# Optimization experiments

Hardware: AMD Instinct MI355X
Metric: run time of the kernel (lower is better)

The kernel has to match this reference:

```python
import jax, jax.numpy as jnp
import numpy as np

S, B, D, H, L = 1024, 2, 1024, 16, 4
HD = D // H            # 64
MLP = 4 * D            # 4096
EPS = 1e-5


def _ln(x, w, b):
    m = x.mean(-1, keepdims=True)
    v = ((x - m) ** 2).mean(-1, keepdims=True)
    return (x - m) * jax.lax.rsqrt(v + EPS) * w + b


def _rotate_half(x):
    h = x.shape[-1] // 2
    return jnp.concatenate([-x[..., h:], x[..., :h]], axis=-1)


def _rope(t, cos, sin):
    # t: (B, S, H, HD); cos/sin: (S, HD) broadcast to (1, S, 1, HD)
    return t * cos[None, :, None, :] + _rotate_half(t) * sin[None, :, None, :]


def setup_inputs() -> dict:
    key = jax.random.key(0)
    ks = iter(jax.random.split(key, 64))

    def p(shape, scale=0.02):
        return jax.random.normal(next(ks), shape, jnp.float32) * scale

    return {
        "x": jax.random.normal(next(ks), (S, B, D), jnp.float32),
        "rotary_pos_emb": jax.random.normal(next(ks), (S, HD // 2), jnp.float32),
        # stacked per-layer params (leading dim L) for lax.scan
        "ln1_w": jnp.ones((L, D), jnp.float32), "ln1_b": jnp.zeros((L, D), jnp.float32),
        "in_w": p((L, 3 * D, D)), "in_b": jnp.zeros((L, 3 * D), jnp.float32),
        "out_w": p((L, D, D)), "out_b": jnp.zeros((L, D), jnp.float32),
        "ln2_w": jnp.ones((L, D), jnp.float32), "ln2_b": jnp.zeros((L, D), jnp.float32),
        "fc_w": p((L, MLP, D)), "fc_b": jnp.zeros((L, MLP), jnp.float32),
        "cp_w": p((L, D, MLP)), "cp_b": jnp.zeros((L, D), jnp.float32),
        # attention pooling head (qkv_bias=False in CrossAttention)
        "pn_q_w": jnp.ones((D,), jnp.float32), "pn_q_b": jnp.zeros((D,), jnp.float32),
        "pn_k_w": jnp.ones((D,), jnp.float32), "pn_k_b": jnp.zeros((D,), jnp.float32),
        "pn_v_w": jnp.ones((D,), jnp.float32), "pn_v_b": jnp.zeros((D,), jnp.float32),
        "pq_w": p((D, D)), "pk_w": p((D, D)), "pv_w": p((D, D)),
        "pp_w": p((D, D)), "pp_b": jnp.zeros((D,), jnp.float32),
    }


def reference(x, rotary_pos_emb, ln1_w, ln1_b, in_w, in_b, out_w, out_b,
              ln2_w, ln2_b, fc_w, fc_b, cp_w, cp_b,
              pn_q_w, pn_q_b, pn_k_w, pn_k_b, pn_v_w, pn_v_b,
              pq_w, pk_w, pv_w, pp_w, pp_b):
    # freqs (S, HD/2) -> cos/sin tiled twice along last dim: (S, HD)
    cos = jnp.tile(jnp.cos(rotary_pos_emb), (1, 2))
    sin = jnp.tile(jnp.sin(rotary_pos_emb), (1, 2))
    scale = 1.0 / np.sqrt(HD).astype(np.float32)

    def layer(h, p):
        l1w, l1b, iw, ib, ow, ob, l2w, l2b, fw, fb, cw, cb = p
        a = _ln(h, l1w, l1b)
        qkv = jnp.einsum('sbd,ed->sbe', a, iw) + ib           # (S,B,3D)
        qkv = qkv.reshape(S, B, 3, H, HD)
        q = jnp.transpose(qkv[:, :, 0], (1, 0, 2, 3))          # (B,S,H,HD)
        k = jnp.transpose(qkv[:, :, 1], (1, 0, 2, 3))
        v = jnp.transpose(qkv[:, :, 2], (1, 0, 2, 3))
        q = _rope(q, cos, sin)
        k = _rope(k, cos, sin)
        q, k, v = (t.transpose(0, 2, 1, 3) for t in (q, k, v))  # (B,H,S,HD)
        attn = jax.nn.softmax(jnp.einsum('bhsd,bhtd->bhst', q, k) * scale, axis=-1)
        o = jnp.einsum('bhst,bhtd->bhsd', attn, v)
        o = o.transpose(2, 0, 1, 3).reshape(S, B, D)           # back to (S,B,D)
        h = h + jnp.einsum('sbd,ed->sbe', o, ow) + ob          # residual + out_proj
        m = _ln(h, l2w, l2b)
        m = jax.nn.gelu(jnp.einsum('sbd,ed->sbe', m, fw) + fb, approximate=False)
        h = h + jnp.einsum('sbe,de->sbd', m, cw) + cb          # residual + c_proj
        return h, None

    h, _ = jax.lax.scan(layer, x, (ln1_w, ln1_b, in_w, in_b, out_w, out_b,
                                   ln2_w, ln2_b, fc_w, fc_b, cp_w, cp_b))

    # AttentionPoolingBlock: mean-pooled single query, cross-attend over tokens
    t = h.transpose(1, 0, 2)                                   # (B,N,C)
    xq = _ln(t.mean(1, keepdims=True), pn_q_w, pn_q_b)         # (B,1,C)
    xk = _ln(t, pn_k_w, pn_k_b)
    xv = _ln(t, pn_v_w, pn_v_b)
    q = (xq @ pq_w.T).reshape(B, 1, H, HD).transpose(0, 2, 1, 3)   # (B,H,1,HD)
    k = (xk @ pk_w.T).reshape(B, S, H, HD).transpose(0, 2, 1, 3)
    v = (xv @ pv_w.T).reshape(B, S, H, HD).transpose(0, 2, 1, 3)
    a = jax.nn.softmax(jnp.einsum('bhqd,bhtd->bhqt', q, k) * scale, axis=-1)
    o = jnp.einsum('bhqt,bhtd->bhqd', a, v).transpose(0, 2, 1, 3).reshape(B, 1, D)
    return (o @ pp_w.T + pp_b)[:, 0]                           # (B, D)
```

## Files before the change

kernel.cpp:

```cpp
#include <hip/hip_runtime.h>
#include <math.h>

#define S_LEN  1024
#define BATCH  2
#define DMODEL 1024
#define NHEAD  16
#define HDIM   64
#define NLAYER 4
#define MLPD   4096
#define MROWS  (S_LEN*BATCH)

typedef __attribute__((ext_vector_type(8))) short bf16x8_t;
typedef __attribute__((ext_vector_type(4))) float f32x4_t;

__device__ __forceinline__ unsigned short f2bf(float f) {
  union { float f; unsigned u; } c; c.f = f;
  return (unsigned short)((c.u + 0x7FFFu + ((c.u >> 16) & 1u)) >> 16);
}
__device__ __forceinline__ float bf2f(unsigned short u) {
  union { unsigned u; float f; } c; c.u = ((unsigned)u) << 16; return c.f;
}

__device__ __forceinline__ void gl_lds16(const unsigned short* g, unsigned short* l) {
  __builtin_amdgcn_global_load_lds(
      (const __attribute__((address_space(1))) unsigned int*)(g),
      (__attribute__((address_space(3))) unsigned int*)(l), 16, 0, 0);
}

template<int CTRL>
__device__ __forceinline__ float dpp16(float x) {
  return __int_as_float(__builtin_amdgcn_update_dpp(
      0, __float_as_int(x), CTRL, 0xf, 0xf, true));
}
__device__ __forceinline__ float rowmax16(float x) {
  x = fmaxf(x, dpp16<0x128>(x));
  x = fmaxf(x, dpp16<0x124>(x));
  x = fmaxf(x, dpp16<0x122>(x));
  x = fmaxf(x, dpp16<0x121>(x));
  return x;
}
__device__ __forceinline__ float rowsum16(float x) {
  x += dpp16<0x128>(x);
  x += dpp16<0x124>(x);
  x += dpp16<0x122>(x);
  x += dpp16<0x121>(x);
  return x;
}

__global__ __launch_bounds__(256) void w2bf_kernel(const float* __restrict__ src,
    unsigned short* __restrict__ dst, int n) {
  const int i = (blockIdx.x * 256 + threadIdx.x) * 8;
  if (i >= n) return;
  float4 v0 = *(const float4*)(src + i);
  float4 v1 = *(const float4*)(src + i + 4);
  ushort4 u0, u1;
  u0.x = f2bf(v0.x); u0.y = f2bf(v0.y); u0.z = f2bf(v0.z); u0.w = f2bf(v0.w);
  u1.x = f2bf(v1.x); u1.y = f2bf(v1.y); u1.z = f2bf(v1.z); u1.w = f2bf(v1.w);
  *(ushort4*)(dst + i)     = u0;
  *(ushort4*)(dst + i + 4) = u1;
}

__global__ __launch_bounds__(256) void trig_kernel(const float* __restrict__ rot,
    float2* __restrict__ tab) {
  const int i = blockIdx.x * 256 + threadIdx.x;
  const float f = rot[i];
  tab[i] = make_float2(cosf(f), sinf(f));
}

template<bool BF16OUT>
__global__ __launch_bounds__(256) void ln_kernel(const float* __restrict__ x,
    const float* __restrict__ w, const float* __restrict__ b,
    void* __restrict__ out, float inscale) {
  const int row = blockIdx.x;
  const int tid = threadIdx.x;
  const float* xr = x + (size_t)row * DMODEL;
  float4 v = *(const float4*)(xr + tid * 4);
  v.x *= inscale; v.y *= inscale; v.z *= inscale; v.w *= inscale;
  float s1 = v.x + v.y + v.z + v.w;
  float s2 = v.x*v.x + v.y*v.y + v.z*v.z + v.w*v.w;
  #pragma unroll
  for (int off = 32; off; off >>= 1) {
    s1 += __shfl_xor(s1, off);
    s2 += __shfl_xor(s2, off);
  }
  __shared__ float as1[4], as2[4];
  if ((tid & 63) == 0) { as1[tid >> 6] = s1; as2[tid >> 6] = s2; }
  __syncthreads();
  s1 = as1[0] + as1[1] + as1[2] + as1[3];
  s2 = as2[0] + as2[1] + as2[2] + as2[3];
  const float mean = s1 * (1.0f / DMODEL);
  const float var  = s2 * (1.0f / DMODEL) - mean * mean;
  const float r = rsqrtf(var + 1e-5f);
  float4 wv = *(const float4*)(w + tid * 4);
  float4 bv = *(const float4*)(b + tid * 4);
  float o0 = (v.x - mean) * r * wv.x + bv.x;
  float o1 = (v.y - mean) * r * wv.y + bv.y;
  float o2 = (v.z - mean) * r * wv.z + bv.z;
  float o3 = (v.w - mean) * r * wv.w + bv.w;
  if (BF16OUT) {
    ushort4 u; u.x = f2bf(o0); u.y = f2bf(o1); u.z = f2bf(o2); u.w = f2bf(o3);
    *(ushort4*)((unsigned short*)out + (size_t)row * DMODEL + tid * 4) = u;
  } else {
    float4 ov; ov.x = o0; ov.y = o1; ov.z = o2; ov.w = o3;
    *(float4*)((float*)out + (size_t)row * DMODEL + tid * 4) = ov;
  }
}

template<int NS, bool ADDDEST, bool DOLN>
__global__ __launch_bounds__(256) void reduce_ln_kernel(
    const float* __restrict__ part, const float* __restrict__ bias,
    float* __restrict__ dest, const float* __restrict__ lnw,
    const float* __restrict__ lnb, unsigned short* __restrict__ lnout) {
  const int row = blockIdx.x;
  const int tid = threadIdx.x;
  const size_t off = (size_t)row * DMODEL + tid * 4;
  float4 v;
  if (ADDDEST) v = *(const float4*)(dest + off);
  else { v.x = 0.f; v.y = 0.f; v.z = 0.f; v.w = 0.f; }
  if (bias) {
    float4 b4 = *(const float4*)(bias + tid * 4);
    v.x += b4.x; v.y += b4.y; v.z += b4.z; v.w += b4.w;
  }
  #pragma unroll
  for (int z = 0; z < NS; ++z) {
    float4 p = *(const float4*)(part + (size_t)z * (MROWS * DMODEL) + off);
    v.x += p.x; v.y += p.y; v.z += p.z; v.w += p.w;
  }
  *(float4*)(dest + off) = v;
  if (DOLN) {
    float s1 = v.x + v.y + v.z + v.w;
    float s2 = v.x*v.x + v.y*v.y + v.z*v.z + v.w*v.w;
    #pragma unroll
    for (int o = 32; o; o >>= 1) {
      s1 += __shfl_xor(s1, o);
      s2 += __shfl_xor(s2, o);
    }
    __shared__ float as1[4], as2[4];
    if ((tid & 63) == 0) { as1[tid >> 6] = s1; as2[tid >> 6] = s2; }
    __syncthreads();
    s1 = as1[0] + as1[1] + as1[2] + as1[3];
    s2 = as2[0] + as2[1] + as2[2] + as2[3];
    const float mean = s1 * (1.0f / DMODEL);
    const float var  = s2 * (1.0f / DMODEL) - mean * mean;
    const float r = rsqrtf(var + 1e-5f);
    float4 wv = *(const float4*)(lnw + tid * 4);
    float4 bv = *(const float4*)(lnb + tid * 4);
    ushort4 u;
    u.x = f2bf((v.x - mean) * r * wv.x + bv.x);
    u.y = f2bf((v.y - mean) * r * wv.y + bv.y);
    u.z = f2bf((v.z - mean) * r * wv.z + bv.z);
    u.w = f2bf((v.w - mean) * r * wv.w + bv.w);
    *(ushort4*)(lnout + (size_t)row * DMODEL + tid * 4) = u;
  }
}

template<int SPLIT, bool GELU, bool PARTIAL, bool OUTBF16>
__global__ __launch_bounds__(256, 3) void gemm_mfma(
    const unsigned short* __restrict__ A, const unsigned short* __restrict__ W,
    const float* __restrict__ bias, void* __restrict__ Cout,
    int M, int N, int K) {
  constexpr int BK = 32;
  __shared__ __align__(16) unsigned short As[2][128 * BK];
  __shared__ __align__(16) unsigned short Bs[2][128 * BK];
  const int tid  = threadIdx.x;
  const int wid  = tid >> 6;
  const int lane = tid & 63;
  const int lrow = lane & 15;
  const int lq   = lane >> 4;

  const int NB = gridDim.x, MB = gridDim.y;
  const int f = blockIdx.y * NB + blockIdx.x;
  const int xcd = f & 7;
  const int idx = f >> 3;
  const int m0 = (idx % MB) * 128;
  const int n0 = (xcd + (idx / MB) * 8) * 128;

  const int wm = (wid >> 1) * 64;
  const int wn = (wid & 1) * 64;
  const int Kc = K / SPLIT;
  const int kbase = blockIdx.z * Kc;

  f32x4_t acc[4][4];
  #pragma unroll
  for (int i = 0; i < 4; ++i)
    #pragma unroll
    for (int j = 0; j < 4; ++j) acc[i][j] = (f32x4_t){0.f, 0.f, 0.f, 0.f};

  const int c1 = tid, c2 = tid + 256;
  const int r1c = c1 >> 2, r2c = c2 >> 2;
  const int kc1 = ((c1 & 3) ^ ((r1c >> 1) & 3)) * 8;
  const int kc2 = ((c2 & 3) ^ ((r2c >> 1) & 3)) * 8;
  const unsigned short* Ag1 = A + (size_t)(m0 + r1c) * K + kbase + kc1;
  const unsigned short* Ag2 = A + (size_t)(m0 + r2c) * K + kbase + kc2;
  const unsigned short* Wg1 = W + (size_t)(n0 + r1c) * K + kbase + kc1;
  const unsigned short* Wg2 = W + (size_t)(n0 + r2c) * K + kbase + kc2;
  const int l1 = c1 * 8, l2 = c2 * 8;

  gl_lds16(Ag1, &As[0][l1]);
  gl_lds16(Ag2, &As[0][l2]);
  gl_lds16(Wg1, &Bs[0][l1]);
  gl_lds16(Wg2, &Bs[0][l2]);
  __syncthreads();

  int cur = 0;
  for (int k0 = 0; k0 < Kc; k0 += BK) {
    if (k0 + BK < Kc) {
      gl_lds16(Ag1 + k0 + BK, &As[cur ^ 1][l1]);
      gl_lds16(Ag2 + k0 + BK, &As[cur ^ 1][l2]);
      gl_lds16(Wg1 + k0 + BK, &Bs[cur ^ 1][l1]);
      gl_lds16(Wg2 + k0 + BK, &Bs[cur ^ 1][l2]);
    }

    bf16x8_t af[4], bfr[4];
    #pragma unroll
    for (int i = 0; i < 4; ++i) {
      const int row = wm + i * 16 + lrow;
      const int ch  = lq ^ ((row >> 1) & 3);
      af[i] = *(const bf16x8_t*)&As[cur][row * BK + ch * 8];
    }
    #pragma unroll
    for (int j = 0; j < 4; ++j) {
      const int row = wn + j * 16 + lrow;
      const int ch  = lq ^ ((row >> 1) & 3);
      bfr[j] = *(const bf16x8_t*)&Bs[cur][row * BK + ch * 8];
    }
    #pragma unroll
    for (int i = 0; i < 4; ++i)
      #pragma unroll
      for (int j = 0; j < 4; ++j)
        acc[i][j] = __builtin_amdgcn_mfma_f32_16x16x32_bf16(af[i], bfr[j], acc[i][j], 0, 0, 0);

    __syncthreads();
    cur ^= 1;
  }

  const size_t zoff = PARTIAL ? (size_t)blockIdx.z * ((size_t)M * N) : 0;
  float bj[4];
  #pragma unroll
  for (int j = 0; j < 4; ++j)
    bj[j] = (bias && (SPLIT == 1 || blockIdx.z == 0)) ? bias[n0 + wn + j * 16 + lrow] : 0.f;
  #pragma unroll
  for (int i = 0; i < 4; ++i) {
    #pragma unroll
    for (int r = 0; r < 4; ++r) {
      const int row = m0 + wm + i * 16 + lq * 4 + r;
      const size_t idx2 = (size_t)row * N + n0 + wn + lrow;
      #pragma unroll
      for (int j = 0; j < 4; ++j) {
        float val = acc[i][j][r] + bj[j];
        if (GELU)
          val = 0.5f * val * (1.0f + erff(val * 0.70710678118654752f));
        if (PARTIAL)
          ((float*)Cout)[zoff + idx2 + j * 16] = val;
        else if (OUTBF16)
          ((unsigned short*)Cout)[idx2 + j * 16] = f2bf(val);
        else
          ((float*)Cout)[idx2 + j * 16] = val;
      }
    }
  }
}

__global__ __launch_bounds__(256) void rope_kernel(const unsigned short* __restrict__ qkv,
    const float2* __restrict__ trig, unsigned short* __restrict__ qt,
    unsigned short* __restrict__ kt) {
  const int idx = blockIdx.x * 256 + threadIdx.x;
  const int d  = idx & 63;
  const int hh = (idx >> 6) & 15;
  const int m  = idx >> 10;
  const int s  = m >> 1;
  const int b  = m & 1;
  const float2 t = trig[s * 32 + (d & 31)];
  const float cs = t.x;
  const float sn = t.y;
  const float sign = (d < 32) ? -1.0f : 1.0f;
  const size_t base  = (size_t)m * 3072 + hh * 64;
  const int bh = b * 16 + hh;
  const size_t obase = (((size_t)bh * 1024 + s) << 6) + d;
  float qv = bf2f(qkv[base + d]);
  float qp = bf2f(qkv[base + (d ^ 32)]);
  qt[obase] = f2bf(qv * cs + sign * qp * sn);
  float kv = bf2f(qkv[base + 1024 + d]);
  float kp = bf2f(qkv[base + 1024 + (d ^ 32)]);
  kt[obase] = f2bf(kv * cs + sign * kp * sn);
}

__global__ __launch_bounds__(256) void vtrans_kernel(const unsigned short* __restrict__ qkv,
    unsigned short* __restrict__ vt) {
  const int bh = blockIdx.x >> 4;
  const int s0 = (blockIdx.x & 15) * 64;
  const int b = bh >> 4, hh = bh & 15;
  __shared__ unsigned short Vl[64 * 72];
  const int t = threadIdx.x;
  const int sl = t >> 2, dcol = (t & 3) * 16;
  const unsigned short* src = qkv + (size_t)((s0 + sl) * 2 + b) * 3072 + 2048 + hh * 64 + dcol;
  uint4 a = *(const uint4*)(src);
  uint4 c = *(const uint4*)(src + 8);
  *(uint4*)&Vl[sl * 72 + dcol]     = a;
  *(uint4*)&Vl[sl * 72 + dcol + 8] = c;
  __syncthreads();
  const int dr = t >> 2, soff = (t & 3) * 16;
  unsigned short o[16];
  #pragma unroll
  for (int i = 0; i < 16; ++i) o[i] = Vl[(soff + i) * 72 + dr];
  unsigned short* dst = vt + (((size_t)bh * 64 + dr) << 10) + s0 + soff;
  *(uint4*)(dst)     = *(uint4*)(o);
  *(uint4*)(dst + 8) = *(uint4*)(o + 8);
}

__global__ __launch_bounds__(256, 3) void attn_kernel(
    const unsigned short* __restrict__ q, const unsigned short* __restrict__ k,
    const unsigned short* __restrict__ vtr, unsigned short* __restrict__ o) {
  const int tid  = threadIdx.x;
  const int wid  = tid >> 6;
  const int lane = tid & 63;
  const int col  = lane & 15;
  const int quad = lane >> 4;
  const int bh   = blockIdx.x >> 4;
  const int qw   = (blockIdx.x & 15) * 64 + wid * 16;

  __shared__ __align__(16) unsigned short Ks[64 * 72];
  __shared__ __align__(16) unsigned short Vs[64 * 72];
  __shared__ __align__(16) unsigned short Pl_[4][16 * 72];
  unsigned short* Pl = Pl_[wid];

  const unsigned short* kb = k   + ((size_t)bh << 16);
  const unsigned short* vb = vtr + ((size_t)bh << 16);

  bf16x8_t qa0, qa1;
  {
    const unsigned short* qp = q + ((((size_t)bh << 10) + qw + col) << 6) + quad * 8;
    qa0 = *(const bf16x8_t*)(qp);
    qa1 = *(const bf16x8_t*)(qp + 32);
  }

  f32x4_t oacc[4];
  #pragma unroll
  for (int j = 0; j < 4; ++j) oacc[j] = (f32x4_t){0.f, 0.f, 0.f, 0.f};
  float mr[4] = {-3.0e38f, -3.0e38f, -3.0e38f, -3.0e38f};
  float lr[4] = {0.f, 0.f, 0.f, 0.f};

  const int srow = tid >> 2;
  const int scol = (tid & 3) * 16;
  const unsigned short* gk0 = kb + (size_t)srow * 64 + scol;
  const unsigned short* gv0 = vb + (size_t)srow * 1024 + scol;
  unsigned short* lk0 = &Ks[srow * 72 + scol];
  unsigned short* lv0 = &Vs[srow * 72 + scol];

  {
    uint4 ka = *(const uint4*)(gk0);
    uint4 kc = *(const uint4*)(gk0 + 8);
    uint4 va = *(const uint4*)(gv0);
    uint4 vc = *(const uint4*)(gv0 + 8);
    *(uint4*)(lk0)     = ka;
    *(uint4*)(lk0 + 8) = kc;
    *(uint4*)(lv0)     = va;
    *(uint4*)(lv0 + 8) = vc;
  }
  __syncthreads();

  for (int t0 = 0; t0 < 1024; t0 += 64) {
    const bool more = (t0 + 64) < 1024;
    uint4 nka, nkc, nva, nvc;
    if (more) {
      const unsigned short* gk = gk0 + (size_t)(t0 + 64) * 64;
      const unsigned short* gv = gv0 + (t0 + 64);
      nka = *(const uint4*)(gk);
      nkc = *(const uint4*)(gk + 8);
      nva = *(const uint4*)(gv);
      nvc = *(const uint4*)(gv + 8);
    }

    f32x4_t sc[4];
    #pragma unroll
    for (int j = 0; j < 4; ++j) {
      bf16x8_t kf0 = *(const bf16x8_t*)&Ks[(j * 16 + col) * 72 + quad * 8];
      bf16x8_t kf1 = *(const bf16x8_t*)&Ks[(j * 16 + col) * 72 + quad * 8 + 32];
      f32x4_t c = (f32x4_t){0.f, 0.f, 0.f, 0.f};
      c = __builtin_amdgcn_mfma_f32_16x16x32_bf16(qa0, kf0, c, 0, 0, 0);
      c = __builtin_amdgcn_mfma_f32_16x16x32_bf16(qa1, kf1, c, 0, 0, 0);
      sc[j] = c;
    }

    #pragma unroll
    for (int r = 0; r < 4; ++r) {
      float s0 = sc[0][r] * 0.125f, s1 = sc[1][r] * 0.125f;
      float s2 = sc[2][r] * 0.125f, s3 = sc[3][r] * 0.125f;
      const float rm = rowmax16(fmaxf(fmaxf(s0, s1), fmaxf(s2, s3)));
      if (__any(rm > mr[r])) {
        const float mn = fmaxf(mr[r], rm);
        const float alpha = __expf(mr[r] - mn);
        mr[r] = mn;
        lr[r] *= alpha;
        #pragma unroll
        for (int j = 0; j < 4; ++j) oacc[j][r] *= alpha;
      }
      const float m = mr[r];
      const float p0 = __expf(s0 - m), p1 = __expf(s1 - m);
      const float p2 = __expf(s2 - m), p3 = __expf(s3 - m);
      lr[r] += rowsum16(p0 + p1 + p2 + p3);
      const int prow = (quad * 4 + r) * 72;
      Pl[prow +  0 + col] = f2bf(p0);
      Pl[prow + 16 + col] = f2bf(p1);
      Pl[prow + 32 + col] = f2bf(p2);
      Pl[prow + 48 + col] = f2bf(p3);
    }

    bf16x8_t pa0 = *(const bf16x8_t*)&Pl[col * 72 + quad * 8];
    bf16x8_t pa1 = *(const bf16x8_t*)&Pl[col * 72 + quad * 8 + 32];
    #pragma unroll
    for (int j = 0; j < 4; ++j) {
      bf16x8_t vf0 = *(const bf16x8_t*)&Vs[(j * 16 + col) * 72 + quad * 8];
      bf16x8_t vf1 = *(const bf16x8_t*)&Vs[(j * 16 + col) * 72 + quad * 8 + 32];
      oacc[j] = __builtin_amdgcn_mfma_f32_16x16x32_bf16(pa0, vf0, oacc[j], 0, 0, 0);
      oacc[j] = __builtin_amdgcn_mfma_f32_16x16x32_bf16(pa1, vf1, oacc[j], 0, 0, 0);
    }

    __syncthreads();
    if (more) {
      *(uint4*)(lk0)     = nka;
      *(uint4*)(lk0 + 8) = nkc;
      *(uint4*)(lv0)     = nva;
      *(uint4*)(lv0 + 8) = nvc;
    }
    __syncthreads();
  }

  const int b = bh >> 4, hh = bh & 15;
  #pragma unroll
  for (int r = 0; r < 4; ++r) {
    const float inv = 1.0f / lr[r];
    const int sq = qw + quad * 4 + r;
    unsigned short* orow = o + (((size_t)sq * 2 + b) << 10) + hh * 64;
    #pragma unroll
    for (int j = 0; j < 4; ++j)
      orow[j * 16 + col] = f2bf(oacc[j][r] * inv);
  }
}

__global__ __launch_bounds__(256) void mean_kernel(const float* __restrict__ h,
    float* __restrict__ tsum) {
  const int idx = blockIdx.x * 256 + threadIdx.x;
  const int bd = idx & 2047;
  const int sc = idx >> 11;
  const int b = bd >> 10, d = bd & 1023;
  float sm = 0.f;
  for (int s = sc * 128; s < sc * 128 + 128; ++s)
    sm += h[(((size_t)s * 2 + b) << 10) + d];
  atomicAdd(&tsum[bd], sm);
}

__global__ __launch_bounds__(256) void smallmv_kernel(const float* __restrict__ in,
    const float* __restrict__ W, const float* __restrict__ bias,
    float* __restrict__ out) {
  const int lane = threadIdx.x & 63;
  const int n = blockIdx.x * 4 + (threadIdx.x >> 6);
  const int b = blockIdx.y;
  const float* wr = W + (size_t)n * 1024;
  const float* xr = in + (size_t)b * 1024;
  float sm = 0.f;
  #pragma unroll
  for (int j = 0; j < 4; ++j) {
    float4 wv = *(const float4*)(wr + lane * 4 + j * 256);
    float4 xv = *(const float4*)(xr + lane * 4 + j * 256);
    sm += wv.x * xv.x + wv.y * xv.y + wv.z * xv.z + wv.w * xv.w;
  }
  #pragma unroll
  for (int off = 32; off; off >>= 1) sm += __shfl_xor(sm, off);
  if (lane == 0) out[(size_t)b * 1024 + n] = sm + (bias ? bias[n] : 0.f);
}

__global__ __launch_bounds__(256) void pool_attn_part(const float* __restrict__ q,
    const float* __restrict__ k, const float* __restrict__ v,
    float* __restrict__ part) {
  const int wid  = (blockIdx.x * 256 + threadIdx.x) >> 6;
  const int lane = threadIdx.x & 63;
  const int bh = wid >> 4, kblk = wid & 15;
  const int b = bh >> 4, hh = bh & 15;
  const float qd = q[(size_t)b * 1024 + hh * 64 + lane];
  float mx = -3.0e38f, l = 0.f, acc = 0.f;
  for (int t = kblk * 64; t < kblk * 64 + 64; ++t) {
    const size_t ro = (((size_t)t * 2 + b) << 10) + hh * 64 + lane;
    float p = qd * k[ro];
    p += __shfl_xor(p, 32); p += __shfl_xor(p, 16); p += __shfl_xor(p, 8);
    p += __shfl_xor(p, 4);  p += __shfl_xor(p, 2);  p += __shfl_xor(p, 1);
    const float sc = p * 0.125f;
    const float mn = fmaxf(mx, sc);
    const float alpha = __expf(mx - mn);
    const float w = __expf(sc - mn);
    acc = acc * alpha + w * v[ro];
    l   = l * alpha + w;
    mx  = mn;
  }
  float* pp = part + (size_t)wid * 68;
  if (lane == 0) { pp[0] = mx; pp[1] = l; }
  pp[4 + lane] = acc;
}

__global__ __launch_bounds__(256) void pool_attn_comb(const float* __restrict__ part,
    float* __restrict__ o) {
  const int wid  = (blockIdx.x * 256 + threadIdx.x) >> 6;
  const int lane = threadIdx.x & 63;
  const float* pb = part + (size_t)wid * 16 * 68;
  float M = -3.0e38f;
  #pragma unroll
  for (int w = 0; w < 16; ++w) M = fmaxf(M, pb[w * 68]);
  float L = 0.f, O = 0.f;
  #pragma unroll
  for (int w = 0; w < 16; ++w) {
    const float e = __expf(pb[w * 68] - M);
    L += e * pb[w * 68 + 1];
    O += e * pb[w * 68 + 4 + lane];
  }
  const int b = wid >> 4, hh = wid & 15;
  o[(size_t)b * 1024 + hh * 64 + lane] = O / L;
}

extern "C" void kernel_launch(void* const* d_in, const int* in_sizes, int n_in,
                              void* d_out, int out_size, void* d_ws, size_t ws_size,
                              hipStream_t stream) {
  (void)in_sizes; (void)n_in; (void)out_size; (void)ws_size;
  const float* x     = (const float*)d_in[0];
  const float* rot   = (const float*)d_in[1];
  const float* ln1_w = (const float*)d_in[2];
  const float* ln1_b = (const float*)d_in[3];
  const float* in_w  = (const float*)d_in[4];
  const float* in_b  = (const float*)d_in[5];
  const float* out_w = (const float*)d_in[6];
  const float* out_b = (const float*)d_in[7];
  const float* ln2_w = (const float*)d_in[8];
  const float* ln2_b = (const float*)d_in[9];
  const float* fc_w  = (const float*)d_in[10];
  const float* fc_b  = (const float*)d_in[11];
  const float* cp_w  = (const float*)d_in[12];
  const float* cp_b  = (const float*)d_in[13];
  const float* pn_q_w = (const float*)d_in[14];
  const float* pn_q_b = (const float*)d_in[15];
  const float* pn_k_w = (const float*)d_in[16];
  const float* pn_k_b = (const float*)d_in[17];
  const float* pn_v_w = (const float*)d_in[18];
  const float* pn_v_b = (const float*)d_in[19];
  const float* pq_w  = (const float*)d_in[20];
  const float* pk_w  = (const float*)d_in[21];
  const float* pv_w  = (const float*)d_in[22];
  const float* pp_w  = (const float*)d_in[23];
  const float* pp_b  = (const float*)d_in[24];

  float* ws = (float*)d_ws;
  const size_t M1 = 1u << 20;
  float* h  = ws;
  float* a  = ws + 2 * M1;
  float* r1 = ws + 4 * M1;
  float* qt = ws + 12 * M1;
  float* kt = ws + 14 * M1;
  float* vt = ws + 16 * M1;
  float* o  = ws + 18 * M1;
  float* trig = ws + 19 * M1;
  float* wbf = ws + 20 * M1;
  unsigned short* a_bf  = (unsigned short*)a;
  unsigned short* r1_bf = (unsigned short*)r1;
  unsigned short* o_bf  = (unsigned short*)o;
  unsigned short* qt_bf = (unsigned short*)qt;
  unsigned short* kt_bf = (unsigned short*)kt;
  unsigned short* vt_bf = (unsigned short*)vt;
  unsigned short* wb_qkv = (unsigned short*)wbf;
  unsigned short* wb_out = wb_qkv + 3145728;
  unsigned short* wb_fc  = wb_out + 1048576;
  unsigned short* wb_cp  = wb_fc  + 4194304;
  float* part_op = r1;
  float* part_cp = qt;
  float* part_pool = ws + 5 * M1;
  float* tsum  = qt;
  float* xq    = qt + 2048;
  float* qpool = qt + 4096;
  float* opool = qt + 6144;
  float* ppart = qt + 8192;

  hipMemcpyAsync(h, x, 2 * M1 * sizeof(float), hipMemcpyDeviceToDevice, stream);

  trig_kernel<<<128, 256, 0, stream>>>(rot, (float2*)trig);
  ln_kernel<true><<<MROWS, 256, 0, stream>>>(h, ln1_w, ln1_b, a_bf, 1.0f);

  for (int l = 0; l < NLAYER; ++l) {
    w2bf_kernel<<<3145728 / 2048, 256, 0, stream>>>(in_w + (size_t)l * 3145728, wb_qkv, 3145728);
    w2bf_kernel<<<1048576 / 2048, 256, 0, stream>>>(out_w + (size_t)l * 1048576, wb_out, 1048576);
    w2bf_kernel<<<4194304 / 2048, 256, 0, stream>>>(fc_w + (size_t)l * 4194304, wb_fc, 4194304);
    w2bf_kernel<<<4194304 / 2048, 256, 0, stream>>>(cp_w + (size_t)l * 4194304, wb_cp, 4194304);

    gemm_mfma<1, false, false, true><<<dim3(3072 / 128, MROWS / 128, 1), 256, 0, stream>>>(
        a_bf, wb_qkv, in_b + l * 3072, r1_bf, MROWS, 3072, 1024);
    rope_kernel<<<8192, 256, 0, stream>>>(r1_bf, (const float2*)trig, qt_bf, kt_bf);
    vtrans_kernel<<<512, 256, 0, stream>>>(r1_bf, vt_bf);
    attn_kernel<<<512, 256, 0, stream>>>(qt_bf, kt_bf, vt_bf, o_bf);
    gemm_mfma<4, false, true, false><<<dim3(1024 / 128, MROWS / 128, 4), 256, 0, stream>>>(
        o_bf, wb_out, nullptr, part_op, MROWS, 1024, 1024);
    reduce_ln_kernel<4, true, true><<<MROWS, 256, 0, stream>>>(
        part_op, out_b + l * 1024, h, ln2_w + l * DMODEL, ln2_b + l * DMODEL, a_bf);
    gemm_mfma<1, true, false, true><<<dim3(4096 / 128, MROWS / 128, 1), 256, 0, stream>>>(
        a_bf, wb_fc, fc_b + l * 4096, r1_bf, MROWS, 4096, 1024);
    gemm_mfma<4, false, true, false><<<dim3(1024 / 128, MROWS / 128, 4), 256, 0, stream>>>(
        r1_bf, wb_cp, nullptr, part_cp, MROWS, 1024, 4096);
    if (l < NLAYER - 1)
      reduce_ln_kernel<4, true, true><<<MROWS, 256, 0, stream>>>(
          part_cp, cp_b + l * 1024, h,
          ln1_w + (l + 1) * DMODEL, ln1_b + (l + 1) * DMODEL, a_bf);
    else
      reduce_ln_kernel<4, true, false><<<MROWS, 256, 0, stream>>>(
          part_cp, cp_b + l * 1024, h, nullptr, nullptr, nullptr);
  }

  hipMemsetAsync(tsum, 0, 2048 * sizeof(float), stream);
  mean_kernel<<<64, 256, 0, stream>>>(h, tsum);
  ln_kernel<false><<<BATCH, 256, 0, stream>>>(tsum, pn_q_w, pn_q_b, xq, 1.0f / S_LEN);
  ln_kernel<true><<<MROWS, 256, 0, stream>>>(h, pn_k_w, pn_k_b, a_bf, 1.0f);
  ln_kernel<true><<<MROWS, 256, 0, stream>>>(h, pn_v_w, pn_v_b, r1_bf, 1.0f);
  smallmv_kernel<<<dim3(256, BATCH), 256, 0, stream>>>(xq, pq_w, nullptr, qpool);
  w2bf_kernel<<<1048576 / 2048, 256, 0, stream>>>(pk_w, wb_qkv, 1048576);
  w2bf_kernel<<<1048576 / 2048, 256, 0, stream>>>(pv_w, wb_out, 1048576);
  gemm_mfma<2, false, true, false><<<dim3(1024 / 128, MROWS / 128, 2), 256, 0, stream>>>(
      a_bf, wb_qkv, nullptr, part_pool, MROWS, 1024, 1024);
  reduce_ln_kernel<2, false, false><<<MROWS, 256, 0, stream>>>(
      part_pool, nullptr, kt, nullptr, nullptr, nullptr);
  gemm_mfma<2, false, true, false><<<dim3(1024 / 128, MROWS / 128, 2), 256, 0, stream>>>(
      r1_bf, wb_out, nullptr, part_pool, MROWS, 1024, 1024);
  reduce_ln_kernel<2, false, false><<<MROWS, 256, 0, stream>>>(
      part_pool, nullptr, vt, nullptr, nullptr, nullptr);
  pool_attn_part<<<128, 256, 0, stream>>>(qpool, kt, vt, ppart);
  pool_attn_comb<<<8, 256, 0, stream>>>(ppart, opool);
  smallmv_kernel<<<dim3(256, BATCH), 256, 0, stream>>>(opool, pp_w, pp_b, (float*)d_out);
}
```

Baseline: 1.072 ms.

## Split attention over key halves with merge kernel, batch weight conversion

The attention kernel now splits the key/value sequence into two halves across a second grid dimension, writing unnormalized partial outputs plus running max/sum. A new merge kernel combines the two halves with log-sum-exp rescaling and writes bf16 output. This doubles the number of attention blocks for more parallelism, at the cost of extra fp32 traffic and an additional launch. Launch bounds are raised to 4 blocks per SM. Weight bf16 conversion is hoisted out of the layer loop into four large launches over all layers, which cuts launch count but needs a larger workspace.

```diff
diff --git a/kernel.cpp b/kernel.cpp
--- a/kernel.cpp
+++ b/kernel.cpp
@@ -308,9 +308,10 @@
   *(uint4*)(dst + 8) = *(uint4*)(o + 8);
 }
 
-__global__ __launch_bounds__(256, 3) void attn_kernel(
+__global__ __launch_bounds__(256, 4) void attn_kernel(
     const unsigned short* __restrict__ q, const unsigned short* __restrict__ k,
-    const unsigned short* __restrict__ vtr, unsigned short* __restrict__ o) {
+    const unsigned short* __restrict__ vtr, float* __restrict__ U,
+    float* __restrict__ ml) {
   const int tid  = threadIdx.x;
   const int wid  = tid >> 6;
   const int lane = tid & 63;
@@ -318,6 +319,8 @@
   const int quad = lane >> 4;
   const int bh   = blockIdx.x >> 4;
   const int qw   = (blockIdx.x & 15) * 64 + wid * 16;
+  const int half = blockIdx.y;
+  const int tbase = half * 512;
 
   __shared__ __align__(16) unsigned short Ks[64 * 72];
   __shared__ __align__(16) unsigned short Vs[64 * 72];
@@ -342,8 +345,8 @@
 
   const int srow = tid >> 2;
   const int scol = (tid & 3) * 16;
-  const unsigned short* gk0 = kb + (size_t)srow * 64 + scol;
-  const unsigned short* gv0 = vb + (size_t)srow * 1024 + scol;
+  const unsigned short* gk0 = kb + (size_t)(tbase + srow) * 64 + scol;
+  const unsigned short* gv0 = vb + (size_t)srow * 1024 + tbase + scol;
   unsigned short* lk0 = &Ks[srow * 72 + scol];
   unsigned short* lv0 = &Vs[srow * 72 + scol];
 
@@ -359,8 +362,8 @@
   }
   __syncthreads();
 
-  for (int t0 = 0; t0 < 1024; t0 += 64) {
-    const bool more = (t0 + 64) < 1024;
+  for (int t0 = 0; t0 < 512; t0 += 64) {
+    const bool more = (t0 + 64) < 512;
     uint4 nka, nkc, nva, nvc;
     if (more) {
       const unsigned short* gk = gk0 + (size_t)(t0 + 64) * 64;
@@ -426,16 +429,38 @@
     __syncthreads();
   }
 
+  const size_t hoff = (size_t)half * (32 * 1024);
+  #pragma unroll
+  for (int r = 0; r < 4; ++r) {
+    const int sq = qw + quad * 4 + r;
+    float* urow = U + (hoff + (size_t)bh * 1024 + sq) * 64;
+    #pragma unroll
+    for (int j = 0; j < 4; ++j)
+      urow[j * 16 + col] = oacc[j][r];
+    if (col == 0) {
+      float2* mp = (float2*)ml + hoff + (size_t)bh * 1024 + sq;
+      *mp = make_float2(mr[r], lr[r]);
+    }
+  }
+}
+
+__global__ __launch_bounds__(256) void attn_merge_kernel(const float* __restrict__ U,
+    const float* __restrict__ ml, unsigned short* __restrict__ o) {
+  const int gw = (blockIdx.x * 256 + threadIdx.x) >> 6;
+  const int lane = threadIdx.x & 63;
+  const int bh = gw >> 10, sq = gw & 1023;
+  const size_t roff = ((size_t)bh * 1024 + sq) * 64;
+  const size_t hstride = (size_t)32 * 1024 * 64;
+  const float u0 = U[roff + lane];
+  const float u1 = U[hstride + roff + lane];
+  const float2 ml0 = ((const float2*)ml)[(size_t)bh * 1024 + sq];
+  const float2 ml1 = ((const float2*)ml)[(size_t)32 * 1024 + bh * 1024 + sq];
+  const float M = fmaxf(ml0.x, ml1.x);
+  const float e0 = __expf(ml0.x - M), e1 = __expf(ml1.x - M);
+  const float L = e0 * ml0.y + e1 * ml1.y;
+  const float val = (u0 * e0 + u1 * e1) / L;
   const int b = bh >> 4, hh = bh & 15;
-  #pragma unroll
-  for (int r = 0; r < 4; ++r) {
-    const float inv = 1.0f / lr[r];
-    const int sq = qw + quad * 4 + r;
-    unsigned short* orow = o + (((size_t)sq * 2 + b) << 10) + hh * 64;
-    #pragma unroll
-    for (int j = 0; j < 4; ++j)
-      orow[j * 16 + col] = f2bf(oacc[j][r] * inv);
-  }
+  o[(((size_t)sq * 2 + b) << 10) + hh * 64 + lane] = f2bf(val);
 }
 
 __global__ __launch_bounds__(256) void mean_kernel(const float* __restrict__ h,
@@ -563,13 +588,15 @@
   unsigned short* qt_bf = (unsigned short*)qt;
   unsigned short* kt_bf = (unsigned short*)kt;
   unsigned short* vt_bf = (unsigned short*)vt;
-  unsigned short* wb_qkv = (unsigned short*)wbf;
-  unsigned short* wb_out = wb_qkv + 3145728;
-  unsigned short* wb_fc  = wb_out + 1048576;
-  unsigned short* wb_cp  = wb_fc  + 4194304;
+  unsigned short* wb_qkv_all = (unsigned short*)wbf;
+  unsigned short* wb_out_all = wb_qkv_all + 12582912;
+  unsigned short* wb_fc_all  = wb_out_all + 4194304;
+  unsigned short* wb_cp_all  = wb_fc_all  + 16777216;
   float* part_op = r1;
   float* part_cp = qt;
   float* part_pool = ws + 5 * M1;
+  float* attn_U  = r1;
+  float* attn_ml = ws + 8 * M1;
   float* tsum  = qt;
   float* xq    = qt + 2048;
   float* qpool = qt + 4096;
@@ -580,18 +607,23 @@
 
   trig_kernel<<<128, 256, 0, stream>>>(rot, (float2*)trig);
   ln_kernel<true><<<MROWS, 256, 0, stream>>>(h, ln1_w, ln1_b, a_bf, 1.0f);
+  w2bf_kernel<<<12582912 / 2048, 256, 0, stream>>>(in_w,  wb_qkv_all, 12582912);
+  w2bf_kernel<<<4194304  / 2048, 256, 0, stream>>>(out_w, wb_out_all, 4194304);
+  w2bf_kernel<<<16777216 / 2048, 256, 0, stream>>>(fc_w,  wb_fc_all,  16777216);
+  w2bf_kernel<<<16777216 / 2048, 256, 0, stream>>>(cp_w,  wb_cp_all,  16777216);
 
   for (int l = 0; l < NLAYER; ++l) {
-    w2bf_kernel<<<3145728 / 2048, 256, 0, stream>>>(in_w + (size_t)l * 3145728, wb_qkv, 3145728);
-    w2bf_kernel<<<1048576 / 2048, 256, 0, stream>>>(out_w + (size_t)l * 1048576, wb_out, 1048576);
-    w2bf_kernel<<<4194304 / 2048, 256, 0, stream>>>(fc_w + (size_t)l * 4194304, wb_fc, 4194304);
-    w2bf_kernel<<<4194304 / 2048, 256, 0, stream>>>(cp_w + (size_t)l * 4194304, wb_cp, 4194304);
+    const unsigned short* wb_qkv = wb_qkv_all + (size_t)l * 3145728;
+    const unsigned short* wb_out = wb_out_all + (size_t)l * 1048576;
+    const unsigned short* wb_fc  = wb_fc_all  + (size_t)l * 4194304;
+    const unsigned short* wb_cp  = wb_cp_all  + (size_t)l * 4194304;
 
     gemm_mfma<1, false, false, true><<<dim3(3072 / 128, MROWS / 128, 1), 256, 0, stream>>>(
         a_bf, wb_qkv, in_b + l * 3072, r1_bf, MROWS, 3072, 1024);
     rope_kernel<<<8192, 256, 0, stream>>>(r1_bf, (const float2*)trig, qt_bf, kt_bf);
     vtrans_kernel<<<512, 256, 0, stream>>>(r1_bf, vt_bf);
-    attn_kernel<<<512, 256, 0, stream>>>(qt_bf, kt_bf, vt_bf, o_bf);
+    attn_kernel<<<dim3(512, 2), 256, 0, stream>>>(qt_bf, kt_bf, vt_bf, attn_U, attn_ml);
+    attn_merge_kernel<<<8192, 256, 0, stream>>>(attn_U, attn_ml, o_bf);
     gemm_mfma<4, false, true, false><<<dim3(1024 / 128, MROWS / 128, 4), 256, 0, stream>>>(
         o_bf, wb_out, nullptr, part_op, MROWS, 1024, 1024);
     reduce_ln_kernel<4, true, true><<<MROWS, 256, 0, stream>>>(
@@ -615,14 +647,16 @@
   ln_kernel<true><<<MROWS, 256, 0, stream>>>(h, pn_k_w, pn_k_b, a_bf, 1.0f);
   ln_kernel<true><<<MROWS, 256, 0, stream>>>(h, pn_v_w, pn_v_b, r1_bf, 1.0f);
   smallmv_kernel<<<dim3(256, BATCH), 256, 0, stream>>>(xq, pq_w, nullptr, qpool);
-  w2bf_kernel<<<1048576 / 2048, 256, 0, stream>>>(pk_w, wb_qkv, 1048576);
-  w2bf_kernel<<<1048576 / 2048, 256, 0, stream>>>(pv_w, wb_out, 1048576);
+  unsigned short* wb_pk = wb_qkv_all;
+  unsigned short* wb_pv = wb_qkv_all + 1048576;
+  w2bf_kernel<<<1048576 / 2048, 256, 0, stream>>>(pk_w, wb_pk, 1048576);
+  w2bf_kernel<<<1048576 / 2048, 256, 0, stream>>>(pv_w, wb_pv, 1048576);
   gemm_mfma<2, false, true, false><<<dim3(1024 / 128, MROWS / 128, 2), 256, 0, stream>>>(
-      a_bf, wb_qkv, nullptr, part_pool, MROWS, 1024, 1024);
+      a_bf, wb_pk, nullptr, part_pool, MROWS, 1024, 1024);
   reduce_ln_kernel<2, false, false><<<MROWS, 256, 0, stream>>>(
       part_pool, nullptr, kt, nullptr, nullptr, nullptr);
   gemm_mfma<2, false, true, false><<<dim3(1024 / 128, MROWS / 128, 2), 256, 0, stream>>>(
-      r1_bf, wb_out, nullptr, part_pool, MROWS, 1024, 1024);
+      r1_bf, wb_pv, nullptr, part_pool, MROWS, 1024, 1024);
   reduce_ln_kernel<2, false, false><<<MROWS, 256, 0, stream>>>(
       part_pool, nullptr, vt, nullptr, nullptr, nullptr);
   pool_attn_part<<<128, 256, 0, stream>>>(qpool, kt, vt, ppart);
```

Measured after the change: 1.077 ms. No clear change (+0.4%).
